# Kernel optimization log

Measured on AMD Instinct MI355X. Metric: run time of the kernel, lower is better.

The kernel has to match this reference:

```python
import jax, jax.numpy as jnp
import numpy as np

B, L, D, DF, E, R = 4, 1024, 1024, 4096, 32768, 64
EPS = 1e-6


def layer_norm(x, g, b, eps=EPS):
    mu = x.mean(-1, keepdims=True)
    var = ((x - mu) ** 2).mean(-1, keepdims=True)
    return (x - mu) * jax.lax.rsqrt(var + eps) * g + b


def setup_inputs() -> dict:
    key = jax.random.key(0)
    ks = jax.random.split(key, 16)
    s = 0.02
    return {
        "hidden_states": jax.random.normal(ks[0], (B, L, D), jnp.float32),
        "rel_table": jax.random.normal(ks[1], (R, D), jnp.float32) * s,
        "Wq": jax.random.normal(ks[2], (D, D), jnp.float32) * s,
        "bq": jnp.zeros((D,), jnp.float32),
        "Wk": jax.random.normal(ks[3], (D, D), jnp.float32) * s,
        "Wv": jax.random.normal(ks[4], (D, D), jnp.float32) * s,
        "Wo": jax.random.normal(ks[5], (D, D), jnp.float32) * s,
        "bo": jnp.zeros((D,), jnp.float32),
        "ln0_g": jnp.ones((D,), jnp.float32),
        "ln0_b": jnp.zeros((D,), jnp.float32),
        "ln1_g": jnp.ones((D,), jnp.float32),
        "ln1_b": jnp.zeros((D,), jnp.float32),
        "W1": jax.random.normal(ks[6], (D, DF), jnp.float32) * s,
        "b1": jnp.zeros((DF,), jnp.float32),
        "W2": jax.random.normal(ks[7], (DF, D), jnp.float32) * s,
        "b2": jnp.zeros((D,), jnp.float32),
        "ln2_g": jnp.ones((D,), jnp.float32),
        "ln2_b": jnp.zeros((D,), jnp.float32),
        "edge_src": jax.random.randint(ks[8], (B, E), 0, L, jnp.int32),
        "edge_dst": jax.random.randint(ks[9], (B, E), 0, L, jnp.int32),
        "edge_rel": jax.random.randint(ks[10], (B, E), 0, R, jnp.int32),
    }


def reference(hidden_states, rel_table, Wq, bq, Wk, Wv, Wo, bo,
              ln0_g, ln0_b, ln1_g, ln1_b, W1, b1, W2, b2, ln2_g, ln2_b,
              edge_src, edge_dst, edge_rel):
    scale = np.sqrt(D).astype(np.float32)  # num_heads=1 -> d_k = D
    hs_norm = layer_norm(hidden_states, ln0_g, ln0_b)

    def rgat_one(x, src, dst, rel):
        # x: [L, D]; src/dst/rel: [E]
        e = rel_table[rel]                       # [E, D] relation embeddings
        q = x @ Wq + bq
        k = x @ Wk
        v = x @ Wv
        score = jnp.sum((k[src] + e) * q[dst], axis=-1) / scale      # [E]
        score = jnp.exp(jnp.clip(score, -10.0, 10.0))
        wv = jax.ops.segment_sum((v[src] + e) * score[:, None], dst, num_segments=L)
        z = jax.ops.segment_sum(score, dst, num_segments=L)          # [L]
        o = wv / z[:, None]
        out = layer_norm(x + o @ Wo + bo, ln1_g, ln1_b)
        ffn = jnp.maximum(out @ W1 + b1, 0.0) @ W2 + b2
        return layer_norm(out + ffn, ln2_g, ln2_b)

    graph_rep = jax.vmap(rgat_one)(hs_norm, edge_src, edge_dst, edge_rel)
    out = jax.nn.elu(graph_rep)                  # dropout = identity (eval)
    return hidden_states + out
```

## Files before the change

kernel.cpp:

```cpp
#include <hip/hip_runtime.h>
#include <hip/hip_bf16.h>

#define B_SZ 4
#define L_SEQ 1024
#define D_MODEL 1024
#define DF_FF 4096
#define E_PER_B 32768
#define R_REL 64
#define M_ROWS (B_SZ * L_SEQ)

typedef __attribute__((ext_vector_type(8))) short bf16x8;
typedef __attribute__((ext_vector_type(4))) float f32x4;

__device__ inline float b2f(unsigned short u) {
    union { unsigned int i; float f; } x; x.i = ((unsigned int)u) << 16; return x.f;
}
__device__ inline unsigned short f2b(float f) {
    union { float f; unsigned int u; } x; x.f = f;
    unsigned int r = x.u + 0x7FFFu + ((x.u >> 16) & 1u);
    return (unsigned short)(r >> 16);
}

#define GLOBAL_CAST(p) ((const __attribute__((address_space(1))) void*)(p))
#define LDS_CAST(p)    ((__attribute__((address_space(3))) void*)(p))

#define BT_QKV (1024u * 3072u)
#define SEXT_M 1152
#define LDA_WV 1088
#define LDB_WVP 1152
#define BT_WVP (1024u * 1152u)

__global__ void prep_all(const float* __restrict__ Wq, const float* __restrict__ Wk,
                         const float* __restrict__ Wv, const float* __restrict__ Wo,
                         const float* __restrict__ W1, const float* __restrict__ W2,
                         const float* __restrict__ rel, const float* __restrict__ bq,
                         const float* __restrict__ hidden,
                         const float* __restrict__ ln0_g, const float* __restrict__ ln0_b,
                         unsigned short* __restrict__ Wqkv_t, unsigned short* __restrict__ Wo_t,
                         unsigned short* __restrict__ W1_t, unsigned short* __restrict__ W2_t,
                         unsigned short* __restrict__ relbPad,
                         float* __restrict__ bqkv,
                         unsigned short* __restrict__ Xn_b16,
                         float* __restrict__ zeroReg) {
    __shared__ float tile[32][33];
    __shared__ float sb1[4], sb2[4];
    const int id = blockIdx.x, tid = threadIdx.x;
    if (id < 12288) {
        const float* src; unsigned short* dst; int K, N, x, y;
        if (id < 4096) {
            const int seg = id >> 10, t = id & 1023;
            K = 1024; N = 1024; x = t & 31; y = t >> 5;
            src = (seg == 0) ? Wq : (seg == 1) ? Wk : (seg == 2) ? Wv : Wo;
            dst = (seg == 3) ? Wo_t : (Wqkv_t + (size_t)seg * 1048576);
        } else if (id < 8192) {
            const int t = id - 4096; K = 1024; N = 4096; x = t & 127; y = t >> 7;
            src = W1; dst = W1_t;
        } else {
            const int t = id - 8192; K = 4096; N = 1024; x = t & 31; y = t >> 5;
            src = W2; dst = W2_t;
        }
        const int n0 = x * 32, k0 = y * 32, tx = tid & 31, ty = tid >> 5;
#pragma unroll
        for (int r = 0; r < 32; r += 8)
            tile[ty + r][tx] = src[(size_t)(k0 + ty + r) * N + (n0 + tx)];
        __syncthreads();
#pragma unroll
        for (int r = 0; r < 32; r += 8)
            dst[(size_t)(n0 + ty + r) * K + (k0 + tx)] = f2b(tile[tx][ty + r]);
    } else if (id < 12800) {
        const int i = (id - 12288) * 256 + tid;
        relbPad[i] = (i < 65536) ? f2b(rel[i]) : (unsigned short)0;
    } else if (id < 12812) {
        const int i = (id - 12800) * 256 + tid;
        bqkv[i] = (i < 1024) ? bq[i] : 0.0f;
    } else if (id < 16908) {
        const int row = id - 12812, t = tid;
        const size_t base = (size_t)row * 1024 + t * 4;
        float4 xv = *(const float4*)(hidden + base);
        float x0 = xv.x, x1 = xv.y, x2 = xv.z, x3 = xv.w;
        float s = x0 + x1 + x2 + x3;
#pragma unroll
        for (int o = 32; o > 0; o >>= 1) s += __shfl_down(s, o);
        if ((t & 63) == 0) sb1[t >> 6] = s;
        __syncthreads();
        const float mu = (sb1[0] + sb1[1] + sb1[2] + sb1[3]) * (1.0f / 1024.0f);
        const float d0 = x0 - mu, d1 = x1 - mu, d2 = x2 - mu, d3 = x3 - mu;
        float s2 = d0 * d0 + d1 * d1 + d2 * d2 + d3 * d3;
#pragma unroll
        for (int o = 32; o > 0; o >>= 1) s2 += __shfl_down(s2, o);
        if ((t & 63) == 0) sb2[t >> 6] = s2;
        __syncthreads();
        const float var = (sb2[0] + sb2[1] + sb2[2] + sb2[3]) * (1.0f / 1024.0f);
        const float rstd = rsqrtf(var + 1e-6f);
        const float4 gv = *(const float4*)(ln0_g + t * 4);
        const float4 bv = *(const float4*)(ln0_b + t * 4);
        ushort4 ob;
        ob.x = f2b(d0 * rstd * gv.x + bv.x);
        ob.y = f2b(d1 * rstd * gv.y + bv.y);
        ob.z = f2b(d2 * rstd * gv.z + bv.z);
        ob.w = f2b(d3 * rstd * gv.w + bv.w);
        *(ushort4*)(Xn_b16 + base) = ob;
    } else {
        const size_t base = (size_t)(id - 16908) * 4096 + tid * 4;
        const float4 z4 = make_float4(0.f, 0.f, 0.f, 0.f);
#pragma unroll
        for (int j = 0; j < 4; j++)
            *(float4*)(zeroReg + base + j * 1024) = z4;
    }
}

__device__ inline void tile_swizzle(int id, int ntn, int& tm, int& tn) {
    tm = ((id & 7) + ((id >> 3) / ntn) * 8) * 128;
    tn = ((id >> 3) % ntn) * 128;
}
__device__ inline void tsw256(int id, int ntn, int& tm, int& tn) {
    tm = ((id & 7) + ((id >> 3) / ntn) * 8) * 256;
    tn = ((id >> 3) % ntn) * 256;
}

#define GEMM_BODY(GA, LDA_, GB, LDB_, KLEN)                                                 \
    f32x4 acc[4][4];                                                                        \
    _Pragma("unroll") for (int i = 0; i < 4; i++)                                           \
        _Pragma("unroll") for (int j = 0; j < 4; j++) acc[i][j] = (f32x4)0.0f;              \
    for (int k0 = 0; k0 < (KLEN); k0 += 64) {                                               \
        __syncthreads();                                                                    \
        _Pragma("unroll") for (int r = 0; r < 4; ++r) {                                     \
            __builtin_amdgcn_global_load_lds(GLOBAL_CAST((GA) + (size_t)r * 8 * (LDA_)),    \
                LDS_CAST(&lA[(wave * 32 + r * 8) * 64]), 16, 0, 0);                         \
            __builtin_amdgcn_global_load_lds(GLOBAL_CAST((GB) + (size_t)r * 8 * (LDB_)),    \
                LDS_CAST(&lB[(wave * 32 + r * 8) * 64]), 16, 0, 0);                         \
        }                                                                                   \
        (GA) += 64; (GB) += 64;                                                             \
        __builtin_amdgcn_s_waitcnt(0);                                                      \
        __syncthreads();                                                                    \
        _Pragma("unroll") for (int kk = 0; kk < 2; ++kk) {                                  \
            const int cb = kk * 4 + quad;                                                   \
            bf16x8 af[4], bf[4];                                                            \
            _Pragma("unroll") for (int i = 0; i < 4; i++) {                                 \
                const int ra = wm + i * 16 + l16;                                           \
                af[i] = *(const bf16x8*)&lA[ra * 64 + ((cb ^ (ra & 7)) * 8)];               \
                const int rb = wn + i * 16 + l16;                                           \
                bf[i] = *(const bf16x8*)&lB[rb * 64 + ((cb ^ (rb & 7)) * 8)];               \
            }                                                                               \
            _Pragma("unroll") for (int mi = 0; mi < 4; mi++)                                \
                _Pragma("unroll") for (int ni = 0; ni < 4; ni++)                            \
                    acc[mi][ni] = __builtin_amdgcn_mfma_f32_16x16x32_bf16(                  \
                        af[mi], bf[ni], acc[mi][ni], 0, 0, 0);                              \
        }                                                                                   \
    }

#define ST_Aq(bufc, QM, kt) { \
    _Pragma("unroll") for (int j_ = 0; j_ < 2; j_++) { \
        const int u_ = j_ * 8 + wv; \
        const int lr_ = ((u_ >> 3) * 128) + (QM) * 64 + ((u_ & 7) * 8); \
        __builtin_amdgcn_global_load_lds(GLOBAL_CAST(Ag + (size_t)lr_ * lda + (kt) * 64), \
            LDS_CAST(&ls[bufc][0][lr_ * 64]), 16, 0, 0); } }
#define ST_Bq(bufc, QN, kt) { \
    _Pragma("unroll") for (int j_ = 0; j_ < 2; j_++) { \
        const int u_ = j_ * 8 + wv; \
        const int lr_ = ((u_ >> 2) * 64) + (QN) * 32 + ((u_ & 3) * 8); \
        __builtin_amdgcn_global_load_lds(GLOBAL_CAST(Bg + (size_t)lr_ * ldb + (kt) * 64), \
            LDS_CAST(&ls[bufc][1][lr_ * 64]), 16, 0, 0); } }

#define RD_Af(bufc, QM) { \
    _Pragma("unroll") for (int m4_ = 0; m4_ < 4; m4_++) \
        _Pragma("unroll") for (int kk_ = 0; kk_ < 2; kk_++) \
            af[m4_][kk_] = *(const bf16x8*)&ls[bufc][0][ \
                (wm * 128 + (QM) * 64 + m4_ * 16 + l16) * 64 + (((kk_ * 4 + quad) ^ (l16 & 7)) * 8)]; }
#define RD_Bs(SLOT, bufc, QN) { \
    _Pragma("unroll") for (int n2_ = 0; n2_ < 2; n2_++) \
        _Pragma("unroll") for (int kk_ = 0; kk_ < 2; kk_++) \
            SLOT[n2_][kk_] = *(const bf16x8*)&ls[bufc][1][ \
                (wc * 64 + (QN) * 32 + n2_ * 16 + l16) * 64 + (((kk_ * 4 + quad) ^ (l16 & 7)) * 8)]; }

#define VM4 asm volatile("s_waitcnt vmcnt(4)" ::: "memory");
#define VM0 asm volatile("s_waitcnt vmcnt(0)" ::: "memory");

#define MMCL(QM, QN, BS) \
    __builtin_amdgcn_s_setprio(1); \
    _Pragma("unroll") for (int m4_ = 0; m4_ < 4; m4_++) \
        _Pragma("unroll") for (int n2_ = 0; n2_ < 2; n2_++) \
            _Pragma("unroll") for (int kk_ = 0; kk_ < 2; kk_++) \
                acc[(QM) * 4 + m4_][(QN) * 2 + n2_] = __builtin_amdgcn_mfma_f32_16x16x32_bf16( \
                    af[m4_][kk_], BS[n2_][kk_], acc[(QM) * 4 + m4_][(QN) * 2 + n2_], 0, 0, 0); \
    __builtin_amdgcn_s_setprio(0);

#define PH_R(bufc, QM, QN, BS, STMT, POST) { \
    STMT; \
    RD_Af(bufc, QM) \
    asm volatile("s_waitcnt lgkmcnt(0)" ::: "memory"); \
    __builtin_amdgcn_sched_barrier(0); \
    MMCL(QM, QN, BS) \
    POST; \
    __builtin_amdgcn_s_barrier(); }
#define PH_H(bufc, QM, QN, BS, STMT, POST) { \
    STMT; \
    __builtin_amdgcn_sched_barrier(0); \
    MMCL(QM, QN, BS) \
    POST; \
    __builtin_amdgcn_s_barrier(); }

template<bool RELU, bool SPLITK>
__global__ __launch_bounds__(512, 2)
void gemm256(const unsigned short* __restrict__ A, int lda,
             const unsigned short* __restrict__ Bt, int ldb,
             const float* __restrict__ bias,
             unsigned short* __restrict__ C, size_t pstride,
             int N, int Kc, int ntn) {
    __shared__ unsigned short ls[2][2][16384];
    int tile_m, tile_n;
    tsw256(blockIdx.x, ntn, tile_m, tile_n);
    const int t = threadIdx.x;
    const int wv = t >> 6, lane = t & 63;
    const int wm = wv >> 2;
    const int wc = wv & 3;
    const int quad = lane >> 4, l16 = lane & 15;
    const int srow8 = lane >> 3;
    const int schunk = ((lane & 7) ^ srow8) * 8;
    const int z = SPLITK ? blockIdx.z : 0;
    const int kofs = z * Kc;

    const unsigned short* Ag = A + (size_t)(tile_m + srow8) * lda + kofs + schunk;
    const unsigned short* Bg = Bt + (size_t)(tile_n + srow8) * ldb + kofs + schunk;

    f32x4 acc[8][4];
#pragma unroll
    for (int i = 0; i < 8; i++)
#pragma unroll
        for (int j = 0; j < 4; j++) acc[i][j] = (f32x4)0.0f;
    bf16x8 af[4][2], b0f[2][2], b1f[2][2];

    ST_Aq(0, 0, 0) ST_Aq(0, 1, 0) ST_Bq(0, 0, 0) ST_Bq(0, 1, 0)
    ST_Aq(1, 0, 1) ST_Bq(1, 1, 1) ST_Aq(1, 1, 1)
    asm volatile("s_waitcnt vmcnt(6)" ::: "memory");
    __builtin_amdgcn_s_barrier();
    RD_Bs(b0f, 0, 0) RD_Bs(b1f, 0, 1)

    const int NI = Kc >> 7;
    for (int it = 0; it < NI - 1; ++it) {
        const int t1 = 2 * it + 1, s0 = 2 * it + 2, s1 = 2 * it + 3;
        PH_R(0, 0, 0, b0f, ST_Bq(1, 0, t1), )
        PH_H(0, 0, 1, b1f, ST_Aq(0, 0, s0), )
        PH_R(0, 1, 1, b1f, ST_Bq(0, 1, s0), VM4 RD_Bs(b1f, 1, 1))
        PH_H(0, 1, 0, b0f, ST_Aq(0, 1, s0), RD_Bs(b0f, 1, 0))
        PH_R(1, 0, 0, b0f, ST_Bq(0, 0, s0), )
        PH_H(1, 0, 1, b1f, ST_Aq(1, 0, s1), )
        PH_R(1, 1, 1, b1f, ST_Bq(1, 1, s1), VM4 RD_Bs(b1f, 0, 1))
        PH_H(1, 1, 0, b0f, ST_Aq(1, 1, s1), RD_Bs(b0f, 0, 0))
    }
    {
        const int t1 = 2 * NI - 1;
        PH_R(0, 0, 0, b0f, ST_Bq(1, 0, t1), )
        PH_H(0, 0, 1, b1f, , )
        PH_R(0, 1, 1, b1f, , VM0 RD_Bs(b1f, 1, 1))
        PH_H(0, 1, 0, b0f, , RD_Bs(b0f, 1, 0))
        PH_R(1, 0, 0, b0f, , )
        PH_H(1, 0, 1, b1f, , )
        PH_R(1, 1, 1, b1f, , )
        PH_H(1, 1, 0, b0f, , )
    }

    unsigned short* Co = C + (SPLITK ? (size_t)z * pstride : 0);
#pragma unroll
    for (int mi = 0; mi < 8; mi++) {
#pragma unroll
        for (int ni = 0; ni < 4; ni++) {
            const int col = tile_n + wc * 64 + ni * 16 + l16;
            const float bv = (SPLITK && z != 0) ? 0.0f : bias[col];
#pragma unroll
            for (int r = 0; r < 4; r++) {
                const int row = tile_m + wm * 128 + mi * 16 + quad * 4 + r;
                float v = acc[mi][ni][r] + bv;
                if (RELU) v = fmaxf(v, 0.0f);
                Co[(size_t)row * N + col] = f2b(v);
            }
        }
    }
}

__global__ __launch_bounds__(256, 4)
void sext_w(const unsigned short* __restrict__ QKV,
            const unsigned short* __restrict__ relPad,
            const unsigned short* __restrict__ Wo_t,
            unsigned short* __restrict__ Pbase,
            unsigned short* __restrict__ Bwvp, int Kc) {
    __shared__ unsigned short lA[128 * 64];
    __shared__ unsigned short lB[128 * 64];
    const int id = blockIdx.x, t = threadIdx.x;
    const int wave = t >> 6, lane = t & 63;
    const int wm = (wave >> 1) * 64, wn = (wave & 1) * 64;
    const int quad = lane >> 4, l16 = lane & 15;
    const int srow = lane >> 3;
    const int schunk = ((lane & 7) ^ srow) * 8;

    if (id >= 576) {
        const int t2 = id - 576;
        const int b = t2 / 72, rem = t2 % 72;
        const int tile_m = (rem / 9) * 128;
        const int tile_n = (rem % 9) * 128;
        const unsigned short* gA = Wo_t + (size_t)(tile_m + wave * 32 + srow) * 1024 + schunk;
        const int brow = tile_n + wave * 32 + srow;
        const unsigned short* gB;
        size_t ldb;
        if (tile_n < 1024) {
            gB = QKV + (size_t)b * BT_QKV + (size_t)brow * 3072 + 2048 + schunk;
            ldb = 3072;
        } else {
            gB = relPad + (size_t)(brow - 1024) * 1024 + schunk;
            ldb = 1024;
        }
        GEMM_BODY(gA, 1024, gB, ldb, 1024)
        unsigned short* P = Bwvp + (size_t)b * BT_WVP;
#pragma unroll
        for (int mi = 0; mi < 4; mi++) {
#pragma unroll
            for (int ni = 0; ni < 4; ni++) {
                const int col = tile_n + wn + ni * 16 + l16;
#pragma unroll
                for (int r = 0; r < 4; r++) {
                    const int row = tile_m + wm + mi * 16 + quad * 4 + r;
                    P[(size_t)row * LDB_WVP + col] = f2b(acc[mi][ni][r]);
                }
            }
        }
        return;
    }

    const int bx = id % 72, b = (id / 72) & 3, z = id / 288;
    const int tile_m = (bx >> 3) * 128;
    const int tile_n = (bx & 7) * 128;
    const int kofs = z * Kc;
    const int arow = tile_m + wave * 32 + srow;
    const unsigned short* gA;
    size_t lda;
    if (tile_m < 1024) {
        gA = QKV + (size_t)b * BT_QKV + (size_t)arow * 3072 + 1024 + kofs + schunk;
        lda = 3072;
    } else {
        gA = relPad + (size_t)(arow - 1024) * 1024 + kofs + schunk;
        lda = 1024;
    }
    const unsigned short* gB = QKV + (size_t)b * BT_QKV
                                   + (size_t)(tile_n + wave * 32 + srow) * 3072 + kofs + schunk;
    GEMM_BODY(gA, lda, gB, 3072, Kc)
    unsigned short* P = Pbase + ((size_t)z * B_SZ + b) * (SEXT_M * 1024);
#pragma unroll
    for (int mi = 0; mi < 4; mi++) {
#pragma unroll
        for (int ni = 0; ni < 4; ni++) {
            const int col = tile_n + wn + ni * 16 + l16;
#pragma unroll
            for (int r = 0; r < 4; r++) {
                const int row = tile_m + wm + mi * 16 + quad * 4 + r;
                P[(size_t)row * 1024 + col] = f2b(acc[mi][ni][r]);
            }
        }
    }
}

__global__ __launch_bounds__(256, 4)
void gemm_wv_splitk(const unsigned short* __restrict__ A,
                    const unsigned short* __restrict__ Bt,
                    const float* __restrict__ bias,
                    unsigned short* __restrict__ Pbase, size_t pstride) {
    __shared__ unsigned short lA[128 * 64];
    __shared__ unsigned short lB[128 * 64];
    int tile_m, tile_n;
    tile_swizzle(blockIdx.x, 8, tile_m, tile_n);
    const int z = blockIdx.z;
    const int kofs = z * 576;
    const int Kc = z ? 512 : 576;
    const int t = threadIdx.x;
    const int wave = t >> 6, lane = t & 63;
    const int wm = (wave >> 1) * 64, wn = (wave & 1) * 64;
    const int quad = lane >> 4, l16 = lane & 15;
    const int srow = lane >> 3;
    const int schunk = ((lane & 7) ^ srow) * 8;
    const unsigned short* gA = A + (size_t)(tile_m + wave * 32 + srow) * LDA_WV + kofs + schunk;
    const unsigned short* gB = Bt + (size_t)(tile_m >> 10) * BT_WVP
                                  + (size_t)(tile_n + wave * 32 + srow) * LDB_WVP + kofs + schunk;
    GEMM_BODY(gA, LDA_WV, gB, LDB_WVP, Kc)
    unsigned short* P = Pbase + (size_t)z * pstride;
#pragma unroll
    for (int mi = 0; mi < 4; mi++) {
#pragma unroll
        for (int ni = 0; ni < 4; ni++) {
            const int col = tile_n + wn + ni * 16 + l16;
            const float bv = (z == 0) ? bias[col] : 0.0f;
#pragma unroll
            for (int r = 0; r < 4; r++) {
                const int row = tile_m + wm + mi * 16 + quad * 4 + r;
                P[(size_t)row * 1024 + col] = f2b(acc[mi][ni][r] + bv);
            }
        }
    }
}

template<bool FINAL, int NR>
__global__ void ln_kernel(const unsigned short* __restrict__ Xb,
                          const unsigned short* __restrict__ Rbase, size_t rstride,
                          const float* __restrict__ g, const float* __restrict__ be,
                          unsigned short* __restrict__ ob16,
                          const float* __restrict__ hidden, float* __restrict__ fout) {
    __shared__ float sb1[4], sb2[4];
    const int row = blockIdx.x, t = threadIdx.x;
    const size_t base = (size_t)row * 1024 + t * 4;

    ushort4 xv = *(const ushort4*)(Xb + base);
    float x0 = b2f(xv.x), x1 = b2f(xv.y), x2 = b2f(xv.z), x3 = b2f(xv.w);
#pragma unroll
    for (int r = 0; r < NR; r++) {
        ushort4 rv = *(const ushort4*)(Rbase + r * rstride + base);
        x0 += b2f(rv.x); x1 += b2f(rv.y); x2 += b2f(rv.z); x3 += b2f(rv.w);
    }
    float s = x0 + x1 + x2 + x3;
#pragma unroll
    for (int o = 32; o > 0; o >>= 1) s += __shfl_down(s, o);
    if ((t & 63) == 0) sb1[t >> 6] = s;
    __syncthreads();
    const float mu = (sb1[0] + sb1[1] + sb1[2] + sb1[3]) * (1.0f / 1024.0f);

    const float d0 = x0 - mu, d1 = x1 - mu, d2 = x2 - mu, d3 = x3 - mu;
    float s2 = d0 * d0 + d1 * d1 + d2 * d2 + d3 * d3;
#pragma unroll
    for (int o = 32; o > 0; o >>= 1) s2 += __shfl_down(s2, o);
    if ((t & 63) == 0) sb2[t >> 6] = s2;
    __syncthreads();
    const float var = (sb2[0] + sb2[1] + sb2[2] + sb2[3]) * (1.0f / 1024.0f);
    const float rstd = rsqrtf(var + 1e-6f);

    const float4 gv = *(const float4*)(g + t * 4);
    const float4 bv = *(const float4*)(be + t * 4);
    const float y0 = d0 * rstd * gv.x + bv.x;
    const float y1 = d1 * rstd * gv.y + bv.y;
    const float y2 = d2 * rstd * gv.z + bv.z;
    const float y3 = d3 * rstd * gv.w + bv.w;

    if (!FINAL) {
        ushort4 ob; ob.x = f2b(y0); ob.y = f2b(y1); ob.z = f2b(y2); ob.w = f2b(y3);
        *(ushort4*)(ob16 + base) = ob;
    } else {
        const float4 hv = *(const float4*)(hidden + base);
        const float e0 = y0 > 0.0f ? y0 : expm1f(y0);
        const float e1 = y1 > 0.0f ? y1 : expm1f(y1);
        const float e2 = y2 > 0.0f ? y2 : expm1f(y2);
        const float e3 = y3 > 0.0f ? y3 : expm1f(y3);
        float4 o; o.x = hv.x + e0; o.y = hv.y + e1; o.z = hv.z + e2; o.w = hv.w + e3;
        *(float4*)(fout + base) = o;
    }
}

__global__ void edge_scatter(const unsigned short* __restrict__ S,
                             const int* __restrict__ src, const int* __restrict__ dst,
                             const int* __restrict__ rel,
                             float* __restrict__ A, float* __restrict__ G) {
    const size_t ZSTR = (size_t)B_SZ * SEXT_M * 1024;
    const int gg = blockIdx.x * 256 + threadIdx.x;
    const int b = gg >> 15;
    const int s = src[gg], d = dst[gg], r = rel[gg];
    const size_t sbase = ((size_t)b * SEXT_M + s) * 1024 + d;
    const size_t tbase = ((size_t)b * SEXT_M + 1024 + r) * 1024 + d;
    const float sval = b2f(S[sbase]) + b2f(S[sbase + ZSTR]);
    const float tval = b2f(S[tbase]) + b2f(S[tbase + ZSTR]);
    float sc = (sval + tval) * (1.0f / 32.0f);
    sc = expf(fminf(fmaxf(sc, -10.0f), 10.0f));
    atomicAdd(&A[((size_t)((b << 10) + d) << 10) + s], sc);
    atomicAdd(&G[((size_t)((b << 10) + d) << 6) + r], sc);
}

__global__ void normalize(const float* __restrict__ A, const float* __restrict__ G,
                          unsigned short* __restrict__ Awv) {
    __shared__ float sInv;
    const int row = blockIdx.x, t = threadIdx.x;
    float v = 0.0f;
    if (t < 64) {
        v = G[(size_t)row * 64 + t];
        float s = v;
#pragma unroll
        for (int o = 1; o < 64; o <<= 1) s += __shfl_xor(s, o);
        if (t == 0) sInv = 1.0f / s;
    }
    __syncthreads();
    const float inv = sInv;
    const size_t obase = (size_t)row * LDA_WV;
    const float4 a = *(const float4*)(A + (size_t)row * 1024 + t * 4);
    ushort4 o;
    o.x = f2b(a.x * inv); o.y = f2b(a.y * inv); o.z = f2b(a.z * inv); o.w = f2b(a.w * inv);
    *(ushort4*)(Awv + obase + t * 4) = o;
    if (t < 16) {
        const float4 gq = *(const float4*)(G + (size_t)row * 64 + t * 4);
        ushort4 og;
        og.x = f2b(gq.x * inv); og.y = f2b(gq.y * inv);
        og.z = f2b(gq.z * inv); og.w = f2b(gq.w * inv);
        *(ushort4*)(Awv + obase + 1024 + t * 4) = og;
    }
}

extern "C" void kernel_launch(void* const* d_in, const int* in_sizes, int n_in,
                              void* d_out, int out_size, void* d_ws, size_t ws_size,
                              hipStream_t stream) {
    const float* hidden  = (const float*)d_in[0];
    const float* rel_tbl = (const float*)d_in[1];
    const float* Wq = (const float*)d_in[2];
    const float* bq = (const float*)d_in[3];
    const float* Wk = (const float*)d_in[4];
    const float* Wv = (const float*)d_in[5];
    const float* Wo = (const float*)d_in[6];
    const float* bo = (const float*)d_in[7];
    const float* ln0_g = (const float*)d_in[8];
    const float* ln0_b = (const float*)d_in[9];
    const float* ln1_g = (const float*)d_in[10];
    const float* ln1_b = (const float*)d_in[11];
    const float* W1 = (const float*)d_in[12];
    const float* b1 = (const float*)d_in[13];
    const float* W2 = (const float*)d_in[14];
    const float* b2 = (const float*)d_in[15];
    const float* ln2_g = (const float*)d_in[16];
    const float* ln2_b = (const float*)d_in[17];
    const int* esrc = (const int*)d_in[18];
    const int* edst = (const int*)d_in[19];
    const int* erel = (const int*)d_in[20];
    float* out = (float*)d_out;

    char* ws = (char*)d_ws;
    const size_t MB = 1024 * 1024;
    unsigned short* Xn_b16  = (unsigned short*)(ws + 16 * MB);
    unsigned short* H1      = (unsigned short*)(ws + 0);
    unsigned short* Wqkv_t  = (unsigned short*)(ws + 24 * MB);
    unsigned short* Wo_t    = (unsigned short*)(ws + 30 * MB);
    unsigned short* W1_t    = (unsigned short*)(ws + 32 * MB);
    unsigned short* W2_t    = (unsigned short*)(ws + 40 * MB);
    unsigned short* relbPad = (unsigned short*)(ws + 48 * MB);
    float*          bqkv    = (float*)(ws + 48 * MB + 512 * 1024);
    unsigned short* QKV     = (unsigned short*)(ws + 49 * MB);
    unsigned short* Awv     = (unsigned short*)(ws + 49 * MB);
    unsigned short* Qw2H    = (unsigned short*)(ws + 49 * MB);
    unsigned short* PwoH    = (unsigned short*)(ws + 66 * MB);
    unsigned short* SxH     = (unsigned short*)(ws + 73 * MB);
    unsigned short* Bwvp    = (unsigned short*)(ws + 92 * MB);
    float*          Amat    = (float*)(ws + 101 * MB);
    float*          Gmat    = (float*)(ws + 117 * MB);
    unsigned short* Out_b16 = (unsigned short*)(ws + 113 * MB);

    const size_t PSTRIDE_H = 4u * 1024 * 1024;
    const dim3 blk(256);
    const dim3 blk512(512);

    prep_all<<<17996, blk, 0, stream>>>(Wq, Wk, Wv, Wo, W1, W2, rel_tbl, bq,
                                        hidden, ln0_g, ln0_b,
                                        Wqkv_t, Wo_t, W1_t, W2_t, relbPad, bqkv,
                                        Xn_b16, Amat);
    gemm256<false, false><<<dim3(192), blk512, 0, stream>>>(
        Xn_b16, 1024, Wqkv_t, 1024, bqkv, QKV, 0, 3072, 1024, 12);
    sext_w<<<864, blk, 0, stream>>>(QKV, relbPad, Wo_t, SxH, Bwvp, 512);
    edge_scatter<<<512, blk, 0, stream>>>(SxH, esrc, edst, erel, Amat, Gmat);
    normalize<<<M_ROWS, blk, 0, stream>>>(Amat, Gmat, Awv);
    gemm_wv_splitk<<<dim3(256, 1, 2), blk, 0, stream>>>(Awv, Bwvp, bo, PwoH, PSTRIDE_H);
    ln_kernel<false, 2><<<M_ROWS, blk, 0, stream>>>(Xn_b16, PwoH, PSTRIDE_H, ln1_g, ln1_b,
                                                    Out_b16, nullptr, nullptr);
    gemm256<true, false><<<dim3(256), blk512, 0, stream>>>(
        Out_b16, 1024, W1_t, 1024, b1, H1, 0, 4096, 1024, 16);
    gemm256<false, true><<<dim3(64, 1, 4), blk512, 0, stream>>>(
        H1, 4096, W2_t, 4096, b2, Qw2H, PSTRIDE_H, 1024, 1024, 4);
    ln_kernel<true, 4><<<M_ROWS, blk, 0, stream>>>(Out_b16, Qw2H, PSTRIDE_H, ln2_g, ln2_b,
                                                   nullptr, hidden, out);
    (void)in_sizes; (void)n_in; (void)out_size; (void)ws_size;
}
```

Baseline: 348.2 us.

## Restructure GEMM main loop into single-tile double-buffered four-phase pipeline

Replaces the two-tile-per-iteration eight-phase schedule with a one-K-tile-per-iteration loop of four phases that prefetch the next tile into the alternate LDS buffer. Each phase issues its LDS fragment reads before a barrier and waits on partial lgkm/vm counters, so global-to-LDS copies overlap MFMA work with a simpler dependency pattern. The prologue now loads only one tile and waits fully. In exchange, the prefetch distance shrinks to one tile and each phase carries an extra barrier, which may expose more memory latency.

```diff
diff --git a/kernel.cpp b/kernel.cpp
--- a/kernel.cpp
+++ b/kernel.cpp
@@ -173,8 +173,9 @@
             SLOT[n2_][kk_] = *(const bf16x8*)&ls[bufc][1][ \
                 (wc * 64 + (QN) * 32 + n2_ * 16 + l16) * 64 + (((kk_ * 4 + quad) ^ (l16 & 7)) * 8)]; }
 
-#define VM4 asm volatile("s_waitcnt vmcnt(4)" ::: "memory");
+#define VM2 asm volatile("s_waitcnt vmcnt(2)" ::: "memory");
 #define VM0 asm volatile("s_waitcnt vmcnt(0)" ::: "memory");
+#define LG8 asm volatile("s_waitcnt lgkmcnt(8)" ::: "memory");
 
 #define MMCL(QM, QN, BS) \
     __builtin_amdgcn_s_setprio(1); \
@@ -185,19 +186,15 @@
                     af[m4_][kk_], BS[n2_][kk_], acc[(QM) * 4 + m4_][(QN) * 2 + n2_], 0, 0, 0); \
     __builtin_amdgcn_s_setprio(0);
 
-#define PH_R(bufc, QM, QN, BS, STMT, POST) { \
+#define PH2(STMT, READS, LGPRE, QM, QN, BS, VMW) { \
     STMT; \
-    RD_Af(bufc, QM) \
+    READS; \
+    LGPRE; \
+    __builtin_amdgcn_s_barrier(); \
     asm volatile("s_waitcnt lgkmcnt(0)" ::: "memory"); \
     __builtin_amdgcn_sched_barrier(0); \
     MMCL(QM, QN, BS) \
-    POST; \
-    __builtin_amdgcn_s_barrier(); }
-#define PH_H(bufc, QM, QN, BS, STMT, POST) { \
-    STMT; \
-    __builtin_amdgcn_sched_barrier(0); \
-    MMCL(QM, QN, BS) \
-    POST; \
+    VMW; \
     __builtin_amdgcn_s_barrier(); }
 
 template<bool RELU, bool SPLITK>
@@ -230,34 +227,24 @@
         for (int j = 0; j < 4; j++) acc[i][j] = (f32x4)0.0f;
     bf16x8 af[4][2], b0f[2][2], b1f[2][2];
 
-    ST_Aq(0, 0, 0) ST_Aq(0, 1, 0) ST_Bq(0, 0, 0) ST_Bq(0, 1, 0)
-    ST_Aq(1, 0, 1) ST_Bq(1, 1, 1) ST_Aq(1, 1, 1)
-    asm volatile("s_waitcnt vmcnt(6)" ::: "memory");
+    ST_Aq(0, 0, 0) ST_Bq(0, 0, 0) ST_Bq(0, 1, 0) ST_Aq(0, 1, 0)
+    VM0
     __builtin_amdgcn_s_barrier();
-    RD_Bs(b0f, 0, 0) RD_Bs(b1f, 0, 1)
-
-    const int NI = Kc >> 7;
-    for (int it = 0; it < NI - 1; ++it) {
-        const int t1 = 2 * it + 1, s0 = 2 * it + 2, s1 = 2 * it + 3;
-        PH_R(0, 0, 0, b0f, ST_Bq(1, 0, t1), )
-        PH_H(0, 0, 1, b1f, ST_Aq(0, 0, s0), )
-        PH_R(0, 1, 1, b1f, ST_Bq(0, 1, s0), VM4 RD_Bs(b1f, 1, 1))
-        PH_H(0, 1, 0, b0f, ST_Aq(0, 1, s0), RD_Bs(b0f, 1, 0))
-        PH_R(1, 0, 0, b0f, ST_Bq(0, 0, s0), )
-        PH_H(1, 0, 1, b1f, ST_Aq(1, 0, s1), )
-        PH_R(1, 1, 1, b1f, ST_Bq(1, 1, s1), VM4 RD_Bs(b1f, 0, 1))
-        PH_H(1, 1, 0, b0f, ST_Aq(1, 1, s1), RD_Bs(b0f, 0, 0))
+
+    const int NT = Kc >> 6;
+    for (int tt = 0; tt < NT - 1; ++tt) {
+        const int c = tt & 1, nb = c ^ 1;
+        PH2(ST_Aq(nb, 0, tt + 1), RD_Af(c, 0) RD_Bs(b0f, c, 0), LG8, 0, 0, b0f, VM2)
+        PH2(ST_Bq(nb, 0, tt + 1), RD_Bs(b1f, c, 1),            ,    0, 1, b1f, VM2)
+        PH2(ST_Bq(nb, 1, tt + 1), RD_Af(c, 1),                 ,    1, 1, b1f, VM2)
+        PH2(ST_Aq(nb, 1, tt + 1), ,                            ,    1, 0, b0f, VM2)
     }
     {
-        const int t1 = 2 * NI - 1;
-        PH_R(0, 0, 0, b0f, ST_Bq(1, 0, t1), )
-        PH_H(0, 0, 1, b1f, , )
-        PH_R(0, 1, 1, b1f, , VM0 RD_Bs(b1f, 1, 1))
-        PH_H(0, 1, 0, b0f, , RD_Bs(b0f, 1, 0))
-        PH_R(1, 0, 0, b0f, , )
-        PH_H(1, 0, 1, b1f, , )
-        PH_R(1, 1, 1, b1f, , )
-        PH_H(1, 1, 0, b0f, , )
+        const int c = (NT - 1) & 1;
+        PH2(, RD_Af(c, 0) RD_Bs(b0f, c, 0), LG8, 0, 0, b0f, VM0)
+        PH2(, RD_Bs(b1f, c, 1),            ,    0, 1, b1f, )
+        PH2(, RD_Af(c, 1),                 ,    1, 1, b1f, )
+        PH2(, ,                            ,    1, 0, b0f, )
     }
 
     unsigned short* Co = C + (SPLITK ? (size_t)z * pstride : 0);
```

Result: no change. 349.9 us (median of 2 runs) (+0.5%).
